# Kernel tuning notes

Hardware: AMD Instinct MI355X
Metric: run time of the kernel (lower is better)

Reference implementation:

```python
import jax, jax.numpy as jnp
import numpy as np
import math

F_DIM = 64
N_NODES = 2048
N_HEADS = 4
HEAD_DIM = F_DIM // N_HEADS
C_DIM = 8
FUSION_WEIGHT = 1e-05
LN_EPS = 1e-5
BATCH = 4


def setup_inputs() -> dict:
    key = jax.random.key(0)
    ks = jax.random.split(key, 16)

    def xavier(k, shape):
        fan_in, fan_out = shape[-2], shape[-1]
        lim = math.sqrt(6.0 / (fan_in + fan_out))
        return jax.random.uniform(k, shape, jnp.float32, -lim, lim)

    return {
        "features": jax.random.normal(ks[0], (BATCH, N_NODES, F_DIM), jnp.float32),
        "fixed_graph": jax.random.uniform(ks[1], (N_NODES, N_NODES), jnp.float32),
        "learned_graph": jax.random.uniform(ks[2], (BATCH, N_NODES, N_NODES), jnp.float32),
        # qkv_compress: Linear(F, 3C); qkv_expand: Linear(3C, 3F)
        "Wqc": xavier(ks[3], (F_DIM, 3 * C_DIM)),
        "bqc": jnp.zeros((3 * C_DIM,), jnp.float32),
        "Wqe": xavier(ks[4], (3 * C_DIM, 3 * F_DIM)),
        "bqe": jnp.zeros((3 * F_DIM,), jnp.float32),
        # output_compress: Linear(F, C); output_expand: Linear(C, F)
        "Woc": xavier(ks[5], (F_DIM, C_DIM)),
        "boc": jnp.zeros((C_DIM,), jnp.float32),
        "Woe": xavier(ks[6], (C_DIM, F_DIM)),
        "boe": jnp.zeros((F_DIM,), jnp.float32),
        # learned structure bias factors [H,N,C] @ [H,C,N]
        "bf1": xavier(ks[7], (N_HEADS, N_NODES, C_DIM)),
        "bf2": xavier(ks[8], (N_HEADS, C_DIM, N_NODES)),
        "graph_fusion": jnp.array([0.5], jnp.float32),
        "ln_g": jnp.ones((F_DIM,), jnp.float32),
        "ln_b": jnp.zeros((F_DIM,), jnp.float32),
    }


def _layernorm(x, g, b):
    mu = jnp.mean(x, axis=-1, keepdims=True)
    var = jnp.mean(jnp.square(x - mu), axis=-1, keepdims=True)
    return (x - mu) * jax.lax.rsqrt(var + LN_EPS) * g + b


def reference(features, fixed_graph, learned_graph, Wqc, bqc, Wqe, bqe,
              Woc, boc, Woe, boe, bf1, bf2, graph_fusion, ln_g, ln_b):
    B, N, F = features.shape
    H, hd = N_HEADS, HEAD_DIM
    residual = features

    # compressed QKV projection: [B,N,F] -> [B,N,3C] -> [B,N,3F]
    qkv = (features @ Wqc + bqc) @ Wqe + bqe
    q, k, v = jnp.split(qkv, 3, axis=-1)
    # [B,N,F] -> [B,H,N,hd]
    to_heads = lambda x: x.reshape(B, N, H, hd).transpose(0, 2, 1, 3)
    q, k, v = to_heads(q), to_heads(k), to_heads(v)

    # attention scores + learned low-rank structure bias [H,N,N]
    scores = jnp.einsum("bhnd,bhmd->bhnm", q, k) / math.sqrt(hd)
    scores = scores + jnp.einsum("hnc,hcm->hnm", bf1, bf2)

    # graph fusion: sigmoid-weighted blend of learned and fixed graphs
    fr = jax.nn.sigmoid(graph_fusion[0])
    combined = fr * learned_graph + (1.0 - fr) * fixed_graph[None, :, :]  # [B,N,N]
    scores = scores + combined[:, None, :, :]

    attn = jax.nn.softmax(scores, axis=-1)  # dropout is identity in eval mode
    context = jnp.einsum("bhnm,bhmd->bhnd", attn, v)
    context = context.transpose(0, 2, 1, 3).reshape(B, N, F)

    out = (context @ Woc + boc) @ Woe + boe
    out = _layernorm(out + residual, ln_g, ln_b)

    reg_loss = FUSION_WEIGHT * jnp.mean(jnp.abs(attn))
    return out, reg_loss
```

## Files before the change

### kernel.cpp

```cpp
#include <hip/hip_runtime.h>
#include <hip/hip_bf16.h>

#define BB 4
#define NN 2048
#define NH 4
#define HDD 16
#define FD 64
#define QB 32
#define SPLIT 8
#define KPB (NN / SPLIT)
#define KT (KPB / 64)
#define CS 68
#define L2E 1.44269504088896f

typedef __attribute__((ext_vector_type(8))) short bf16x8;
typedef __attribute__((ext_vector_type(4))) float f32x4;

union BW { __hip_bfloat16 b; unsigned short u; };

static __device__ inline unsigned pk2(float a, float b) {
    BW x, y;
    x.b = __float2bfloat16(a);
    y.b = __float2bfloat16(b);
    return (unsigned)x.u | ((unsigned)y.u << 16);
}

static __device__ inline float wsum(float v) {
    v += __shfl_xor(v, 1);  v += __shfl_xor(v, 2);  v += __shfl_xor(v, 4);
    v += __shfl_xor(v, 8);  v += __shfl_xor(v, 16); v += __shfl_xor(v, 32);
    return v;
}

__global__ __launch_bounds__(256) void fuse_kernel(
    const float* __restrict__ Wqc, const float* __restrict__ bqc,
    const float* __restrict__ Wqe, const float* __restrict__ bqe,
    const float* __restrict__ Woc, const float* __restrict__ boc,
    const float* __restrict__ Woe, const float* __restrict__ boe,
    float* __restrict__ W1, float* __restrict__ b1,
    float* __restrict__ W2, float* __restrict__ b2)
{
    const int t = threadIdx.x;
    if (blockIdx.x == 0) {
        for (int idx = t; idx < 64 * 192; idx += 256) {
            const int r = idx / 192, c = idx - r * 192;
            float a = 0.f;
            #pragma unroll
            for (int j = 0; j < 24; ++j) a += Wqc[r * 24 + j] * Wqe[j * 192 + c];
            if (c < 64) a *= 0.25f * L2E;
            W1[idx] = a;
        }
        if (t < 192) {
            float a = bqe[t];
            #pragma unroll
            for (int j = 0; j < 24; ++j) a += bqc[j] * Wqe[j * 192 + t];
            if (t < 64) a *= 0.25f * L2E;
            b1[t] = a;
        }
    } else {
        for (int idx = t; idx < 64 * 64; idx += 256) {
            const int r = idx >> 6, c = idx & 63;
            float a = 0.f;
            #pragma unroll
            for (int j = 0; j < 8; ++j) a += Woc[r * 8 + j] * Woe[j * 64 + c];
            W2[idx] = a;
        }
        if (t < 64) {
            float a = boe[t];
            #pragma unroll
            for (int j = 0; j < 8; ++j) a += boc[j] * Woe[j * 64 + t];
            b2[t] = a;
        }
    }
}

__global__ __launch_bounds__(256) void qkv_kernel(
    const float* __restrict__ feat,
    const float* __restrict__ W1, const float* __restrict__ b1,
    const float* __restrict__ bf1, const float* __restrict__ bf2,
    __hip_bfloat16* __restrict__ Qe, __hip_bfloat16* __restrict__ Ke,
    __hip_bfloat16* __restrict__ Vt)
{
    __shared__ float fl[4][64];
    const int t = threadIdx.x;
    const int w = t >> 6, lane = t & 63;
    const int bn = blockIdx.x * 4 + w;
    const int b = bn >> 11, n = bn & (NN - 1);

    fl[w][lane] = feat[(size_t)bn * FD + lane];
    __syncthreads();

    float v0 = b1[lane], v1 = b1[lane + 64], v2 = b1[lane + 128];
    #pragma unroll 8
    for (int d = 0; d < 64; ++d) {
        const float f = fl[w][d];
        v0 += f * W1[d * 192 + lane];
        v1 += f * W1[d * 192 + 64 + lane];
        v2 += f * W1[d * 192 + 128 + lane];
    }

    const int h = lane >> 4, hi = lane & 15;
    const size_t rowQ = (((size_t)b * NH + h) * NN + n) * 32;
    Qe[rowQ + hi] = __float2bfloat16(v0);
    Ke[rowQ + hi] = __float2bfloat16(v1);
    Vt[(((size_t)b * NH + h) * HDD + hi) * NN + n] = __float2bfloat16(v2);

    if (lane < 32) {
        const int hh = lane >> 3, c = lane & 7;
        const size_t r = (((size_t)b * NH + hh) * NN + n) * 32;
        Qe[r + 16 + c] = __float2bfloat16(bf1[((size_t)hh * NN + n) * 8 + c] * L2E);
        Qe[r + 24 + c] = __float2bfloat16(0.f);
    } else {
        const int hh = (lane - 32) >> 3, c = lane & 7;
        const size_t r = (((size_t)b * NH + hh) * NN + n) * 32;
        Ke[r + 16 + c] = __float2bfloat16(bf2[((size_t)hh * 8 + c) * NN + n]);
        Ke[r + 24 + c] = __float2bfloat16(0.f);
    }
}

__global__ __launch_bounds__(256, 4) void attn_kernel(
    const float* __restrict__ fixedg, const float* __restrict__ learng,
    const float* __restrict__ gfus,
    const __hip_bfloat16* __restrict__ Qe, const __hip_bfloat16* __restrict__ Ke,
    const __hip_bfloat16* __restrict__ Vt,
    float* __restrict__ pacc, float* __restrict__ psum)
{
    __shared__ float lds[2 * QB * CS];

    const int bid = blockIdx.x;
    const int split = bid & (SPLIT - 1);
    const int qt = (bid >> 3) & 63;
    const int b = bid >> 9;
    const int qb = qt << 5;
    const int kbase = split * KPB;
    const int t = threadIdx.x;
    const int hw = t >> 6;
    const int lane = t & 63;
    const int ql = lane & 15;
    const int g  = lane >> 4;

    const float sg = 1.f / (1.f + __expf(-gfus[0]));
    const float fre = sg * L2E, ofre = (1.f - sg) * L2E;

    const size_t bhN = ((size_t)b * NH + hw) * NN;
    const bf16x8 qfA = *(const bf16x8*)(Qe + (bhN + qb + ql) * 32 + g * 8);
    const bf16x8 qfB = *(const bf16x8*)(Qe + (bhN + qb + 16 + ql) * 32 + g * 8);
    const __hip_bfloat16* kptr = Ke + bhN * 32;
    const __hip_bfloat16* vbase = Vt + (((size_t)b * NH + hw) * HDD + ql) * NN;
    const int krow = 8 * (ql >> 2) + (ql & 3);

    const int sq = t >> 3;
    const int sk = (t & 7) * 8;
    const float* lrow = learng + ((size_t)b * NN + qb + sq) * NN + kbase + sk;
    const float* frow = fixedg + ((size_t)(qb + sq)) * NN + kbase + sk;

    float ssA = 0.f, ssB = 0.f;
    f32x4 accA = {0.f, 0.f, 0.f, 0.f}, accB = {0.f, 0.f, 0.f, 0.f};
    f32x4 l0, l1, f0, f1;

    l0 = *(const f32x4*)(lrow);      l1 = *(const f32x4*)(lrow + 4);
    f0 = *(const f32x4*)(frow);      f1 = *(const f32x4*)(frow + 4);
    *(f32x4*)&lds[sq * CS + sk]     = fre * l0 + ofre * f0;
    *(f32x4*)&lds[sq * CS + sk + 4] = fre * l1 + ofre * f1;

    #pragma unroll
    for (int kt = 0; kt < KT; ++kt) {
        __syncthreads();
        if (kt + 1 < KT) {
            l0 = *(const f32x4*)(lrow + (kt + 1) * 64);
            l1 = *(const f32x4*)(lrow + (kt + 1) * 64 + 4);
            f0 = *(const f32x4*)(frow + (kt + 1) * 64);
            f1 = *(const f32x4*)(frow + (kt + 1) * 64 + 4);
        }
        const float* cmb = lds + (kt & 1) * (QB * CS);
        #pragma unroll
        for (int hf = 0; hf < 2; ++hf) {
            const int kb = kbase + kt * 64 + hf * 32;
            const bf16x8 k0 = *(const bf16x8*)(kptr + (size_t)(kb + krow) * 32 + g * 8);
            const bf16x8 k1 = *(const bf16x8*)(kptr + (size_t)(kb + 4 + krow) * 32 + g * 8);
            const f32x4 z = {0.f, 0.f, 0.f, 0.f};
            f32x4 cA0 = __builtin_amdgcn_mfma_f32_16x16x32_bf16(k0, qfA, z, 0, 0, 0);
            f32x4 cA1 = __builtin_amdgcn_mfma_f32_16x16x32_bf16(k1, qfA, z, 0, 0, 0);
            f32x4 cB0 = __builtin_amdgcn_mfma_f32_16x16x32_bf16(k0, qfB, z, 0, 0, 0);
            f32x4 cB1 = __builtin_amdgcn_mfma_f32_16x16x32_bf16(k1, qfB, z, 0, 0, 0);
            const int col = hf * 32 + 8 * g;
            const f32x4 gA0 = *(const f32x4*)&cmb[ql * CS + col];
            const f32x4 gA1 = *(const f32x4*)&cmb[ql * CS + col + 4];
            const f32x4 gB0 = *(const f32x4*)&cmb[(ql + 16) * CS + col];
            const f32x4 gB1 = *(const f32x4*)&cmb[(ql + 16) * CS + col + 4];
            #pragma unroll
            for (int j = 0; j < 4; ++j) {
                cA0[j] = __builtin_amdgcn_exp2f(cA0[j] + gA0[j]);
                cA1[j] = __builtin_amdgcn_exp2f(cA1[j] + gA1[j]);
                cB0[j] = __builtin_amdgcn_exp2f(cB0[j] + gB0[j]);
                cB1[j] = __builtin_amdgcn_exp2f(cB1[j] + gB1[j]);
                ssA += cA0[j] + cA1[j];
                ssB += cB0[j] + cB1[j];
            }
            union { unsigned u[4]; bf16x8 v; } pfA, pfB;
            pfA.u[0] = pk2(cA0[0], cA0[1]);  pfA.u[1] = pk2(cA0[2], cA0[3]);
            pfA.u[2] = pk2(cA1[0], cA1[1]);  pfA.u[3] = pk2(cA1[2], cA1[3]);
            pfB.u[0] = pk2(cB0[0], cB0[1]);  pfB.u[1] = pk2(cB0[2], cB0[3]);
            pfB.u[2] = pk2(cB1[0], cB1[1]);  pfB.u[3] = pk2(cB1[2], cB1[3]);
            const bf16x8 vf = *(const bf16x8*)(vbase + kb + 8 * g);
            accA = __builtin_amdgcn_mfma_f32_16x16x32_bf16(vf, pfA.v, accA, 0, 0, 0);
            accB = __builtin_amdgcn_mfma_f32_16x16x32_bf16(vf, pfB.v, accB, 0, 0, 0);
        }
        if (kt + 1 < KT) {
            float* dst = lds + ((kt + 1) & 1) * (QB * CS);
            *(f32x4*)&dst[sq * CS + sk]     = fre * l0 + ofre * f0;
            *(f32x4*)&dst[sq * CS + sk + 4] = fre * l1 + ofre * f1;
        }
    }

    ssA += __shfl_xor(ssA, 16);  ssA += __shfl_xor(ssA, 32);
    ssB += __shfl_xor(ssB, 16);  ssB += __shfl_xor(ssB, 32);
    if (g == 0) {
        psum[((size_t)(split * BB + b) * NH + hw) * NN + qb + ql] = ssA;
        psum[((size_t)(split * BB + b) * NH + hw) * NN + qb + 16 + ql] = ssB;
    }

    float* ldsO = lds;
    #pragma unroll
    for (int j = 0; j < 4; ++j) {
        ldsO[ql * CS + hw * 16 + 4 * g + j] = accA[j];
        ldsO[(ql + 16) * CS + hw * 16 + 4 * g + j] = accB[j];
    }
    __syncthreads();
    {
        const int r = t >> 3, c = (t & 7) * 8;
        const f32x4 o0 = *(const f32x4*)&ldsO[r * CS + c];
        const f32x4 o1 = *(const f32x4*)&ldsO[r * CS + c + 4];
        float* prow = pacc + ((size_t)(split * BB + b) * NN + qb + r) * FD + c;
        *(f32x4*)prow = o0;
        *(f32x4*)(prow + 4) = o1;
    }
}

__global__ __launch_bounds__(256) void out_kernel(
    const float* __restrict__ pacc, const float* __restrict__ psum,
    const float* __restrict__ feat,
    const float* __restrict__ W2, const float* __restrict__ b2,
    const float* __restrict__ lng, const float* __restrict__ lnb,
    float* __restrict__ out)
{
    __shared__ float cl[4][64];
    const int t = threadIdx.x;
    const int w = t >> 6, d = t & 63;
    const int node = blockIdx.x * 4 + w;
    const int b = node >> 11, n = node & (NN - 1);
    const int h = d >> 4;

    float a = 0.f, sh = 0.f;
    #pragma unroll
    for (int sp = 0; sp < SPLIT; ++sp) {
        a  += pacc[((size_t)sp * BB * NN + node) * FD + d];
        sh += psum[((size_t)(sp * BB + b) * NH + h) * NN + n];
    }
    cl[w][d] = a / sh;
    __syncthreads();

    float o = b2[d];
    #pragma unroll 8
    for (int dd = 0; dd < 64; ++dd) o += cl[w][dd] * W2[dd * 64 + d];
    o += feat[(size_t)node * FD + d];

    const float mu = wsum(o) * (1.f / 64.f);
    const float df = o - mu;
    const float va = wsum(df * df) * (1.f / 64.f);
    out[(size_t)node * FD + d] = df * rsqrtf(va + 1e-5f) * lng[d] + lnb[d];
    if (blockIdx.x == 0 && t == 0)
        out[(size_t)BB * NN * FD] = 4.8828125e-9f;
}

extern "C" void kernel_launch(void* const* d_in, const int* in_sizes, int n_in,
                              void* d_out, int out_size, void* d_ws, size_t ws_size,
                              hipStream_t stream) {
    const float* feat   = (const float*)d_in[0];
    const float* fixedg = (const float*)d_in[1];
    const float* learng = (const float*)d_in[2];
    const float* Wqc = (const float*)d_in[3];
    const float* bqc = (const float*)d_in[4];
    const float* Wqe = (const float*)d_in[5];
    const float* bqe = (const float*)d_in[6];
    const float* Woc = (const float*)d_in[7];
    const float* boc = (const float*)d_in[8];
    const float* Woe = (const float*)d_in[9];
    const float* boe = (const float*)d_in[10];
    const float* bf1 = (const float*)d_in[11];
    const float* bf2 = (const float*)d_in[12];
    const float* gfus = (const float*)d_in[13];
    const float* lng = (const float*)d_in[14];
    const float* lnb = (const float*)d_in[15];

    char* ws = (char*)d_ws;
    __hip_bfloat16* Qe = (__hip_bfloat16*)ws;
    __hip_bfloat16* Ke = Qe + (size_t)BB * NH * NN * 32;
    __hip_bfloat16* Vt = Ke + (size_t)BB * NH * NN * 32;
    float* pacc = (float*)(Vt + (size_t)BB * NH * HDD * NN);
    float* psum = pacc + (size_t)SPLIT * BB * NN * FD;
    float* W1 = psum + (size_t)SPLIT * BB * NH * NN;
    float* b1 = W1 + 64 * 192;
    float* W2 = b1 + 192;
    float* b2 = W2 + 64 * 64;
    float* out = (float*)d_out;

    hipLaunchKernelGGL(fuse_kernel, dim3(2), dim3(256), 0, stream,
                       Wqc, bqc, Wqe, bqe, Woc, boc, Woe, boe, W1, b1, W2, b2);
    hipLaunchKernelGGL(qkv_kernel, dim3(BB * NN / 4), dim3(256), 0, stream,
                       feat, W1, b1, bf1, bf2, Qe, Ke, Vt);
    hipLaunchKernelGGL(attn_kernel, dim3(BB * (NN / QB) * SPLIT), dim3(256), 0, stream,
                       fixedg, learng, gfus, Qe, Ke, Vt, pacc, psum);
    hipLaunchKernelGGL(out_kernel, dim3(BB * NN / 4), dim3(256), 0, stream,
                       pacc, psum, feat, W2, b2, lng, lnb, out);
}
```

Baseline: 206.4 us.

## Precompute blended graph bias in fp16 and drop LDS staging in attention

A new kernel blends the learned and fixed graphs once into an fp16 bias tensor, which the attention kernel reads directly from global memory instead of staging fp32 blends through double-buffered LDS with barriers. The key split drops from 8 to 4. The weight-fusion kernel is removed and the low-rank projections are computed inline in the qkv and output kernels. Total memory traffic rises because the intermediate tensor is written and re-read, and fp16 rounding of the bias adds some error.

```diff
diff --git a/kernel.cpp b/kernel.cpp
--- a/kernel.cpp
+++ b/kernel.cpp
@@ -7,14 +7,14 @@
 #define HDD 16
 #define FD 64
 #define QB 32
-#define SPLIT 8
+#define SPLIT 4
 #define KPB (NN / SPLIT)
 #define KT (KPB / 64)
-#define CS 68
 #define L2E 1.44269504088896f
 
 typedef __attribute__((ext_vector_type(8))) short bf16x8;
 typedef __attribute__((ext_vector_type(4))) float f32x4;
+typedef __attribute__((ext_vector_type(8))) _Float16 f16x8;
 
 union BW { __hip_bfloat16 b; unsigned short u; };
 
@@ -31,56 +31,41 @@
     return v;
 }
 
-__global__ __launch_bounds__(256) void fuse_kernel(
+__global__ __launch_bounds__(256) void blend_kernel(
+    const float* __restrict__ learng, const float* __restrict__ fixedg,
+    const float* __restrict__ gfus, _Float16* __restrict__ E)
+{
+    const float sg = 1.f / (1.f + __expf(-gfus[0]));
+    const float fre = sg * L2E, ofre = (1.f - sg) * L2E;
+    const size_t base = ((size_t)blockIdx.x * 256 + threadIdx.x) * 32;
+    #pragma unroll
+    for (int i = 0; i < 32; i += 8) {
+        const size_t o = base + i;
+        const f32x4 l0 = *(const f32x4*)(learng + o);
+        const f32x4 l1 = *(const f32x4*)(learng + o + 4);
+        const size_t fo = o & ((size_t)NN * NN - 1);
+        const f32x4 f0 = *(const f32x4*)(fixedg + fo);
+        const f32x4 f1 = *(const f32x4*)(fixedg + fo + 4);
+        f16x8 e;
+        #pragma unroll
+        for (int j = 0; j < 4; ++j) {
+            e[j]     = (_Float16)(fre * l0[j] + ofre * f0[j]);
+            e[4 + j] = (_Float16)(fre * l1[j] + ofre * f1[j]);
+        }
+        *(f16x8*)(E + o) = e;
+    }
+}
+
+__global__ __launch_bounds__(256) void qkv_kernel(
+    const float* __restrict__ feat,
     const float* __restrict__ Wqc, const float* __restrict__ bqc,
     const float* __restrict__ Wqe, const float* __restrict__ bqe,
-    const float* __restrict__ Woc, const float* __restrict__ boc,
-    const float* __restrict__ Woe, const float* __restrict__ boe,
-    float* __restrict__ W1, float* __restrict__ b1,
-    float* __restrict__ W2, float* __restrict__ b2)
-{
-    const int t = threadIdx.x;
-    if (blockIdx.x == 0) {
-        for (int idx = t; idx < 64 * 192; idx += 256) {
-            const int r = idx / 192, c = idx - r * 192;
-            float a = 0.f;
-            #pragma unroll
-            for (int j = 0; j < 24; ++j) a += Wqc[r * 24 + j] * Wqe[j * 192 + c];
-            if (c < 64) a *= 0.25f * L2E;
-            W1[idx] = a;
-        }
-        if (t < 192) {
-            float a = bqe[t];
-            #pragma unroll
-            for (int j = 0; j < 24; ++j) a += bqc[j] * Wqe[j * 192 + t];
-            if (t < 64) a *= 0.25f * L2E;
-            b1[t] = a;
-        }
-    } else {
-        for (int idx = t; idx < 64 * 64; idx += 256) {
-            const int r = idx >> 6, c = idx & 63;
-            float a = 0.f;
-            #pragma unroll
-            for (int j = 0; j < 8; ++j) a += Woc[r * 8 + j] * Woe[j * 64 + c];
-            W2[idx] = a;
-        }
-        if (t < 64) {
-            float a = boe[t];
-            #pragma unroll
-            for (int j = 0; j < 8; ++j) a += boc[j] * Woe[j * 64 + t];
-            b2[t] = a;
-        }
-    }
-}
-
-__global__ __launch_bounds__(256) void qkv_kernel(
-    const float* __restrict__ feat,
-    const float* __restrict__ W1, const float* __restrict__ b1,
     const float* __restrict__ bf1, const float* __restrict__ bf2,
     __hip_bfloat16* __restrict__ Qe, __hip_bfloat16* __restrict__ Ke,
     __hip_bfloat16* __restrict__ Vt)
 {
     __shared__ float fl[4][64];
+    __shared__ float cc[4][24];
     const int t = threadIdx.x;
     const int w = t >> 6, lane = t & 63;
     const int bn = blockIdx.x * 4 + w;
@@ -89,18 +74,27 @@
     fl[w][lane] = feat[(size_t)bn * FD + lane];
     __syncthreads();
 
-    float v0 = b1[lane], v1 = b1[lane + 64], v2 = b1[lane + 128];
-    #pragma unroll 8
-    for (int d = 0; d < 64; ++d) {
-        const float f = fl[w][d];
-        v0 += f * W1[d * 192 + lane];
-        v1 += f * W1[d * 192 + 64 + lane];
-        v2 += f * W1[d * 192 + 128 + lane];
+    if (t < 96) {
+        const int node = t / 24, j = t - node * 24;
+        float a = bqc[j];
+        #pragma unroll 8
+        for (int d = 0; d < 64; ++d) a += fl[node][d] * Wqc[d * 24 + j];
+        cc[node][j] = a;
+    }
+    __syncthreads();
+
+    float v0 = bqe[lane], v1 = bqe[lane + 64], v2 = bqe[lane + 128];
+    #pragma unroll
+    for (int j = 0; j < 24; ++j) {
+        const float c = cc[w][j];
+        v0 += c * Wqe[j * 192 + lane];
+        v1 += c * Wqe[j * 192 + 64 + lane];
+        v2 += c * Wqe[j * 192 + 128 + lane];
     }
 
     const int h = lane >> 4, hi = lane & 15;
     const size_t rowQ = (((size_t)b * NH + h) * NN + n) * 32;
-    Qe[rowQ + hi] = __float2bfloat16(v0);
+    Qe[rowQ + hi] = __float2bfloat16(v0 * (0.25f * L2E));
     Ke[rowQ + hi] = __float2bfloat16(v1);
     Vt[(((size_t)b * NH + h) * HDD + hi) * NN + n] = __float2bfloat16(v2);
 
@@ -118,18 +112,17 @@
 }
 
 __global__ __launch_bounds__(256, 4) void attn_kernel(
-    const float* __restrict__ fixedg, const float* __restrict__ learng,
-    const float* __restrict__ gfus,
+    const _Float16* __restrict__ E,
     const __hip_bfloat16* __restrict__ Qe, const __hip_bfloat16* __restrict__ Ke,
     const __hip_bfloat16* __restrict__ Vt,
     float* __restrict__ pacc, float* __restrict__ psum)
 {
-    __shared__ float lds[2 * QB * CS];
+    __shared__ float ldsO[QB * 68];
 
     const int bid = blockIdx.x;
     const int split = bid & (SPLIT - 1);
-    const int qt = (bid >> 3) & 63;
-    const int b = bid >> 9;
+    const int qt = (bid >> 2) & 63;
+    const int b = bid >> 8;
     const int qb = qt << 5;
     const int kbase = split * KPB;
     const int t = threadIdx.x;
@@ -138,9 +131,6 @@
     const int ql = lane & 15;
     const int g  = lane >> 4;
 
-    const float sg = 1.f / (1.f + __expf(-gfus[0]));
-    const float fre = sg * L2E, ofre = (1.f - sg) * L2E;
-
     const size_t bhN = ((size_t)b * NH + hw) * NN;
     const bf16x8 qfA = *(const bf16x8*)(Qe + (bhN + qb + ql) * 32 + g * 8);
     const bf16x8 qfB = *(const bf16x8*)(Qe + (bhN + qb + 16 + ql) * 32 + g * 8);
@@ -148,51 +138,33 @@
     const __hip_bfloat16* vbase = Vt + (((size_t)b * NH + hw) * HDD + ql) * NN;
     const int krow = 8 * (ql >> 2) + (ql & 3);
 
-    const int sq = t >> 3;
-    const int sk = (t & 7) * 8;
-    const float* lrow = learng + ((size_t)b * NN + qb + sq) * NN + kbase + sk;
-    const float* frow = fixedg + ((size_t)(qb + sq)) * NN + kbase + sk;
+    const _Float16* erA = E + ((size_t)b * NN + qb + ql) * NN + kbase + 8 * g;
+    const _Float16* erB = erA + (size_t)16 * NN;
 
     float ssA = 0.f, ssB = 0.f;
     f32x4 accA = {0.f, 0.f, 0.f, 0.f}, accB = {0.f, 0.f, 0.f, 0.f};
-    f32x4 l0, l1, f0, f1;
-
-    l0 = *(const f32x4*)(lrow);      l1 = *(const f32x4*)(lrow + 4);
-    f0 = *(const f32x4*)(frow);      f1 = *(const f32x4*)(frow + 4);
-    *(f32x4*)&lds[sq * CS + sk]     = fre * l0 + ofre * f0;
-    *(f32x4*)&lds[sq * CS + sk + 4] = fre * l1 + ofre * f1;
-
-    #pragma unroll
+
+    #pragma unroll 2
     for (int kt = 0; kt < KT; ++kt) {
-        __syncthreads();
-        if (kt + 1 < KT) {
-            l0 = *(const f32x4*)(lrow + (kt + 1) * 64);
-            l1 = *(const f32x4*)(lrow + (kt + 1) * 64 + 4);
-            f0 = *(const f32x4*)(frow + (kt + 1) * 64);
-            f1 = *(const f32x4*)(frow + (kt + 1) * 64 + 4);
-        }
-        const float* cmb = lds + (kt & 1) * (QB * CS);
         #pragma unroll
         for (int hf = 0; hf < 2; ++hf) {
-            const int kb = kbase + kt * 64 + hf * 32;
+            const int co = kt * 64 + hf * 32;
+            const int kb = kbase + co;
             const bf16x8 k0 = *(const bf16x8*)(kptr + (size_t)(kb + krow) * 32 + g * 8);
             const bf16x8 k1 = *(const bf16x8*)(kptr + (size_t)(kb + 4 + krow) * 32 + g * 8);
+            const f16x8 eA = *(const f16x8*)(erA + co);
+            const f16x8 eB = *(const f16x8*)(erB + co);
             const f32x4 z = {0.f, 0.f, 0.f, 0.f};
             f32x4 cA0 = __builtin_amdgcn_mfma_f32_16x16x32_bf16(k0, qfA, z, 0, 0, 0);
             f32x4 cA1 = __builtin_amdgcn_mfma_f32_16x16x32_bf16(k1, qfA, z, 0, 0, 0);
             f32x4 cB0 = __builtin_amdgcn_mfma_f32_16x16x32_bf16(k0, qfB, z, 0, 0, 0);
             f32x4 cB1 = __builtin_amdgcn_mfma_f32_16x16x32_bf16(k1, qfB, z, 0, 0, 0);
-            const int col = hf * 32 + 8 * g;
-            const f32x4 gA0 = *(const f32x4*)&cmb[ql * CS + col];
-            const f32x4 gA1 = *(const f32x4*)&cmb[ql * CS + col + 4];
-            const f32x4 gB0 = *(const f32x4*)&cmb[(ql + 16) * CS + col];
-            const f32x4 gB1 = *(const f32x4*)&cmb[(ql + 16) * CS + col + 4];
             #pragma unroll
             for (int j = 0; j < 4; ++j) {
-                cA0[j] = __builtin_amdgcn_exp2f(cA0[j] + gA0[j]);
-                cA1[j] = __builtin_amdgcn_exp2f(cA1[j] + gA1[j]);
-                cB0[j] = __builtin_amdgcn_exp2f(cB0[j] + gB0[j]);
-                cB1[j] = __builtin_amdgcn_exp2f(cB1[j] + gB1[j]);
+                cA0[j] = __builtin_amdgcn_exp2f(cA0[j] + (float)eA[j]);
+                cA1[j] = __builtin_amdgcn_exp2f(cA1[j] + (float)eA[4 + j]);
+                cB0[j] = __builtin_amdgcn_exp2f(cB0[j] + (float)eB[j]);
+                cB1[j] = __builtin_amdgcn_exp2f(cB1[j] + (float)eB[4 + j]);
                 ssA += cA0[j] + cA1[j];
                 ssB += cB0[j] + cB1[j];
             }
@@ -205,11 +177,6 @@
             accA = __builtin_amdgcn_mfma_f32_16x16x32_bf16(vf, pfA.v, accA, 0, 0, 0);
             accB = __builtin_amdgcn_mfma_f32_16x16x32_bf16(vf, pfB.v, accB, 0, 0, 0);
         }
-        if (kt + 1 < KT) {
-            float* dst = lds + ((kt + 1) & 1) * (QB * CS);
-            *(f32x4*)&dst[sq * CS + sk]     = fre * l0 + ofre * f0;
-            *(f32x4*)&dst[sq * CS + sk + 4] = fre * l1 + ofre * f1;
-        }
     }
 
     ssA += __shfl_xor(ssA, 16);  ssA += __shfl_xor(ssA, 32);
@@ -219,17 +186,16 @@
         psum[((size_t)(split * BB + b) * NH + hw) * NN + qb + 16 + ql] = ssB;
     }
 
-    float* ldsO = lds;
     #pragma unroll
     for (int j = 0; j < 4; ++j) {
-        ldsO[ql * CS + hw * 16 + 4 * g + j] = accA[j];
-        ldsO[(ql + 16) * CS + hw * 16 + 4 * g + j] = accB[j];
+        ldsO[ql * 68 + hw * 16 + 4 * g + j] = accA[j];
+        ldsO[(ql + 16) * 68 + hw * 16 + 4 * g + j] = accB[j];
     }
     __syncthreads();
     {
         const int r = t >> 3, c = (t & 7) * 8;
-        const f32x4 o0 = *(const f32x4*)&ldsO[r * CS + c];
-        const f32x4 o1 = *(const f32x4*)&ldsO[r * CS + c + 4];
+        const f32x4 o0 = *(const f32x4*)&ldsO[r * 68 + c];
+        const f32x4 o1 = *(const f32x4*)&ldsO[r * 68 + c + 4];
         float* prow = pacc + ((size_t)(split * BB + b) * NN + qb + r) * FD + c;
         *(f32x4*)prow = o0;
         *(f32x4*)(prow + 4) = o1;
@@ -239,11 +205,13 @@
 __global__ __launch_bounds__(256) void out_kernel(
     const float* __restrict__ pacc, const float* __restrict__ psum,
     const float* __restrict__ feat,
-    const float* __restrict__ W2, const float* __restrict__ b2,
+    const float* __restrict__ Woc, const float* __restrict__ boc,
+    const float* __restrict__ Woe, const float* __restrict__ boe,
     const float* __restrict__ lng, const float* __restrict__ lnb,
     float* __restrict__ out)
 {
     __shared__ float cl[4][64];
+    __shared__ float co[4][8];
     const int t = threadIdx.x;
     const int w = t >> 6, d = t & 63;
     const int node = blockIdx.x * 4 + w;
@@ -259,9 +227,18 @@
     cl[w][d] = a / sh;
     __syncthreads();
 
-    float o = b2[d];
-    #pragma unroll 8
-    for (int dd = 0; dd < 64; ++dd) o += cl[w][dd] * W2[dd * 64 + d];
+    if (t < 32) {
+        const int nd = t >> 3, j = t & 7;
+        float s = boc[j];
+        #pragma unroll 8
+        for (int dd = 0; dd < 64; ++dd) s += cl[nd][dd] * Woc[dd * 8 + j];
+        co[nd][j] = s;
+    }
+    __syncthreads();
+
+    float o = boe[d];
+    #pragma unroll
+    for (int j = 0; j < 8; ++j) o += co[w][j] * Woe[j * 64 + d];
     o += feat[(size_t)node * FD + d];
 
     const float mu = wsum(o) * (1.f / 64.f);
@@ -296,20 +273,17 @@
     __hip_bfloat16* Qe = (__hip_bfloat16*)ws;
     __hip_bfloat16* Ke = Qe + (size_t)BB * NH * NN * 32;
     __hip_bfloat16* Vt = Ke + (size_t)BB * NH * NN * 32;
-    float* pacc = (float*)(Vt + (size_t)BB * NH * HDD * NN);
+    _Float16* E = (_Float16*)(Vt + (size_t)BB * NH * HDD * NN);
+    float* pacc = (float*)(E + (size_t)BB * NN * NN);
     float* psum = pacc + (size_t)SPLIT * BB * NN * FD;
-    float* W1 = psum + (size_t)SPLIT * BB * NH * NN;
-    float* b1 = W1 + 64 * 192;
-    float* W2 = b1 + 192;
-    float* b2 = W2 + 64 * 64;
     float* out = (float*)d_out;
 
-    hipLaunchKernelGGL(fuse_kernel, dim3(2), dim3(256), 0, stream,
-                       Wqc, bqc, Wqe, bqe, Woc, boc, Woe, boe, W1, b1, W2, b2);
+    hipLaunchKernelGGL(blend_kernel, dim3(BB * NN * NN / (256 * 32)), dim3(256), 0, stream,
+                       learng, fixedg, gfus, E);
     hipLaunchKernelGGL(qkv_kernel, dim3(BB * NN / 4), dim3(256), 0, stream,
-                       feat, W1, b1, bf1, bf2, Qe, Ke, Vt);
+                       feat, Wqc, bqc, Wqe, bqe, bf1, bf2, Qe, Ke, Vt);
     hipLaunchKernelGGL(attn_kernel, dim3(BB * (NN / QB) * SPLIT), dim3(256), 0, stream,
-                       fixedg, learng, gfus, Qe, Ke, Vt, pacc, psum);
+                       E, Qe, Ke, Vt, pacc, psum);
     hipLaunchKernelGGL(out_kernel, dim3(BB * NN / 4), dim3(256), 0, stream,
-                       pacc, psum, feat, W2, b2, lng, lnb, out);
-}
+                       pacc, psum, feat, Woc, boc, Woe, boe, lng, lnb, out);
+}
```

New measurement: 220.6 us. 6.9% more time.
